# Kernel tuning notes

Hardware: AMD Instinct MI355X
Metric: run time of the kernel (lower is better)

Reference implementation:

```python
import jax, jax.numpy as jnp
import numpy as np

B, S, IN_DIM, H, NH, DH, OUT_DIM, K, N_KB, L, DFF = 32, 128, 1024, 1024, 8, 128, 256, 10, 500000, 2, 2048


def setup_inputs() -> dict:
    key = jax.random.key(0)
    ks = jax.random.split(key, 16)
    def rn(k, shape, scale=0.02):
        return jax.random.normal(k, shape, jnp.float32) * scale
    return {
        "x": jax.random.normal(ks[0], (B, S, IN_DIM), jnp.float32),
        "ctx": jax.random.normal(ks[1], (B, 1, IN_DIM), jnp.float32),
        "indices": jax.random.randint(ks[2], (B, S, K), 0, N_KB),
        "KB_embs": jax.random.normal(ks[3], (N_KB, OUT_DIM), jnp.float32),
        "W_in": rn(ks[4], (IN_DIM, H)), "b_in": jnp.zeros((H,), jnp.float32),
        "Wqkv": rn(ks[5], (L, H, 3 * H)), "bqkv": jnp.zeros((L, 3 * H), jnp.float32),
        "Wo": rn(ks[6], (L, H, H)), "bo": jnp.zeros((L, H), jnp.float32),
        "ln1_g": jnp.ones((L, H), jnp.float32), "ln1_b": jnp.zeros((L, H), jnp.float32),
        "W1": rn(ks[7], (L, H, DFF)), "b1": jnp.zeros((L, DFF), jnp.float32),
        "W2": rn(ks[8], (L, DFF, H)), "b2": jnp.zeros((L, H), jnp.float32),
        "ln2_g": jnp.ones((L, H), jnp.float32), "ln2_b": jnp.zeros((L, H), jnp.float32),
        "W_out": rn(ks[9], (H, OUT_DIM)), "b_out": jnp.zeros((OUT_DIM,), jnp.float32),
        "ds_W1": rn(ks[10], (OUT_DIM, OUT_DIM)), "ds_b1": jnp.zeros((OUT_DIM,), jnp.float32),
        "ds_W2": rn(ks[11], (OUT_DIM, 1)), "ds_b2": jnp.zeros((1,), jnp.float32),
        "cs_W1": rn(ks[12], (OUT_DIM, OUT_DIM)), "cs_b1": jnp.zeros((OUT_DIM,), jnp.float32),
        "cs_W2": rn(ks[13], (OUT_DIM, 1)), "cs_b2": jnp.zeros((1,), jnp.float32),
    }


def _ln(x, g, b, eps=1e-5):
    m = x.mean(-1, keepdims=True)
    v = ((x - m) ** 2).mean(-1, keepdims=True)
    return (x - m) * jax.lax.rsqrt(v + eps) * g + b


def _encoder_layer(h, Wqkv, bqkv, Wo, bo, g1, bn1, W1, b1, W2, b2, g2, bn2):
    # h: (Sq, Bt, H). PyTorch default batch_first=False -> axis 0 is the attended
    # sequence axis (here the data batch axis B, exactly as the original code runs).
    Sq, Bt, Hd = h.shape
    q, k, v = jnp.split(h @ Wqkv + bqkv, 3, axis=-1)
    q = q.reshape(Sq, Bt, NH, DH)
    k = k.reshape(Sq, Bt, NH, DH)
    v = v.reshape(Sq, Bt, NH, DH)
    att = jnp.einsum('sbhd,tbhd->bhst', q, k) * (1.0 / (DH ** 0.5))
    att = jax.nn.softmax(att, axis=-1)
    o = jnp.einsum('bhst,tbhd->sbhd', att, v).reshape(Sq, Bt, Hd)
    h = _ln(h + o @ Wo + bo, g1, bn1)          # post-norm, eps=1e-5
    ff = jax.nn.relu(h @ W1 + b1) @ W2 + b2    # default dim_feedforward=2048, relu
    return _ln(h + ff, g2, bn2)


def _forward(x, ctx, indices, KB_embs, W_in, b_in, Wqkv, bqkv, Wo, bo, ln1_g, ln1_b,
             W1, b1, W2, b2, ln2_g, ln2_b, W_out, b_out,
             ds_W1, ds_b1, ds_W2, ds_b2, cs_W1, cs_b1, cs_W2, cs_b2):
    h = jnp.concatenate([ctx, x], axis=1)          # (B, S+1, in_dim)
    h = jax.nn.relu(h @ W_in + b_in)               # mapper head (dropout off in eval)
    for l in range(Wqkv.shape[0]):
        h = _encoder_layer(h, Wqkv[l], bqkv[l], Wo[l], bo[l], ln1_g[l], ln1_b[l],
                           W1[l], b1[l], W2[l], b2[l], ln2_g[l], ln2_b[l])
    out = h @ W_out + b_out                        # (B, S+1, out_dim)
    ctx_e, pred = out[:, :1], out[:, 1:]
    idx = jnp.where(indices < 0, 0, indices)       # indices[indices == -1] = 0
    cand = KB_embs[idx]                            # (B, S, K, out_dim) gather
    d = cand - pred[:, :, None, :]
    c = ctx_e[:, :, None, :] * cand
    ds = jax.nn.relu(d @ ds_W1 + ds_b1) @ ds_W2 + ds_b2   # distance_score (B,S,K,1)
    cs = jax.nn.relu(c @ cs_W1 + cs_b1) @ cs_W2 + cs_b2   # context_score: computed but unused by original output
    del cs
    cand_out = jnp.concatenate([ds, cand], axis=-1)       # (B, S, K, 1+out_dim)
    return pred, cand_out


def reference(x, ctx, indices, KB_embs, W_in, b_in, Wqkv, bqkv, Wo, bo, ln1_g, ln1_b,
              W1, b1, W2, b2, ln2_g, ln2_b, W_out, b_out,
              ds_W1, ds_b1, ds_W2, ds_b2, cs_W1, cs_b1, cs_W2, cs_b2):
    return _forward(x, ctx, indices, KB_embs, W_in, b_in, Wqkv, bqkv, Wo, bo,
                    ln1_g, ln1_b, W1, b1, W2, b2, ln2_g, ln2_b, W_out, b_out,
                    ds_W1, ds_b1, ds_W2, ds_b2, cs_W1, cs_b1, cs_W2, cs_b2)
```

## Files before the change

### kernel.cpp

```cpp
#include <hip/hip_runtime.h>
#include <hip/hip_bf16.h>

typedef __attribute__((ext_vector_type(4))) float f32x4;
typedef __attribute__((ext_vector_type(8))) short s16x8;
typedef __attribute__((ext_vector_type(4))) unsigned short u16x4;

#define B_      32
#define S_      128
#define SEQ     129
#define IN_DIM  1024
#define HD      1024
#define NHEAD   8
#define DH      128
#define OUT_DIM 256
#define KC      10
#define DFF     2048
#define MROWS   (B_*SEQ)
#define MPAD    4224
#define NCAND   (B_*S_*KC)

__device__ __forceinline__ short f2bf(float f) {
  unsigned u = __builtin_bit_cast(unsigned, f);
  u += 0x7FFFu + ((u >> 16) & 1u);
  return (short)(u >> 16);
}
__device__ __forceinline__ float bf2f(short s) {
  return __builtin_bit_cast(float, ((unsigned)(unsigned short)s) << 16);
}
__device__ __forceinline__ void gload16(const short* g, short* l) {
  __builtin_amdgcn_global_load_lds(
      (const __attribute__((address_space(1))) unsigned*)g,
      (__attribute__((address_space(3))) unsigned*)l, 16, 0, 0);
}

__global__ __launch_bounds__(256) void transpose_all(
    const float* __restrict__ W_in,  const float* __restrict__ Wqkv,
    const float* __restrict__ Wo,    const float* __restrict__ W1,
    const float* __restrict__ W2,    const float* __restrict__ W_out,
    const float* __restrict__ dsW1,
    short* __restrict__ WinT,  short* __restrict__ WqkvT,
    short* __restrict__ WoT,   short* __restrict__ W1T,
    short* __restrict__ W2T,   short* __restrict__ WoutT,
    short* __restrict__ dsW1T) {
  const int b = blockIdx.x;
  const float* src; short* dst; int K, N, local;
  if (b < 1024)       { src = W_in;  dst = WinT;  K = 1024; N = 1024; local = b; }
  else if (b < 7168)  { int l = (b - 1024) / 3072; local = (b - 1024) % 3072;
                        src = Wqkv + (size_t)l * 1024 * 3072;
                        dst = WqkvT + (size_t)l * 3072 * 1024; K = 1024; N = 3072; }
  else if (b < 9216)  { int l = (b - 7168) / 1024; local = (b - 7168) % 1024;
                        src = Wo + (size_t)l * 1024 * 1024;
                        dst = WoT + (size_t)l * 1024 * 1024; K = 1024; N = 1024; }
  else if (b < 13312) { int l = (b - 9216) / 2048; local = (b - 9216) % 2048;
                        src = W1 + (size_t)l * 1024 * 2048;
                        dst = W1T + (size_t)l * 2048 * 1024; K = 1024; N = 2048; }
  else if (b < 17408) { int l = (b - 13312) / 2048; local = (b - 13312) % 2048;
                        src = W2 + (size_t)l * 2048 * 1024;
                        dst = W2T + (size_t)l * 1024 * 2048; K = 2048; N = 1024; }
  else if (b < 17664) { local = b - 17408; src = W_out; dst = WoutT; K = 1024; N = 256; }
  else                { local = b - 17664; src = dsW1;  dst = dsW1T; K = 256;  N = 256; }
  const int tilesX = N >> 5;
  const int n0 = (local % tilesX) << 5, k0 = (local / tilesX) << 5;

  __shared__ float tile[32][33];
  const int tx = threadIdx.x & 31, ty = threadIdx.x >> 5;
#pragma unroll
  for (int i = 0; i < 4; ++i)
    tile[ty + i * 8][tx] = src[(size_t)(k0 + ty + i * 8) * N + n0 + tx];
  __syncthreads();
#pragma unroll
  for (int i = 0; i < 4; ++i)
    dst[(size_t)(n0 + ty + i * 8) * K + k0 + tx] = f2bf(tile[tx][ty + i * 8]);
}

template <int EPI, bool SPLIT, typename OutT>
__global__ __launch_bounds__(256) void gemm_bt(const short* __restrict__ A,
                                               const short* __restrict__ Bt,
                                               const float* __restrict__ bias,
                                               OutT* __restrict__ C,
                                               float* __restrict__ P,
                                               int M, int N, int K,
                                               int gm, int gn, int groupM,
                                               int kper) {
  __shared__ alignas(16) short As0[4096], As1[4096];
  __shared__ alignas(16) short Bs0[4096], Bs1[4096];
  const int tid = threadIdx.x;
  const int lane = tid & 63, wave = tid >> 6;
  const int wr = wave >> 1, wc = wave & 1;

  const int nwg = gm * gn;
  int orig = blockIdx.x;
  int split = 0;
  if constexpr (SPLIT) { split = orig / nwg; orig %= nwg; }
  const int xcd = orig & 7, kk = orig >> 3;
  const int q = nwg >> 3, r = nwg & 7;
  const int wg = (xcd < r ? xcd * (q + 1) : r * (q + 1) + (xcd - r) * q) + kk;
  const int tpg = groupM * gn;
  const int grp = wg / tpg, rem = wg % tpg;
  const int g0 = grp * groupM;
  const int gsz = (groupM < gm - g0) ? groupM : (gm - g0);
  const int bm = (g0 + rem % gsz) * 128;
  const int bn = (rem / gsz) * 128;
  const int kbase = SPLIT ? split * kper : 0;

  const short* pa[2];
  const short* pb[2];
#pragma unroll
  for (int i = 0; i < 2; ++i) {
    const int idx = i * 256 + tid;
    const int rr = idx >> 2, ss = idx & 3, gg = ss ^ ((rr >> 1) & 3);
    pa[i] = A + (size_t)(bm + rr) * K + kbase + gg * 8;
    pb[i] = Bt + (size_t)(bn + rr) * K + kbase + gg * 8;
  }

  auto stage = [&](short* aBuf, short* bBuf, int t) {
    const int kofs = t << 5;
    gload16(pa[0] + kofs, aBuf + wave * 512);
    gload16(pa[1] + kofs, aBuf + 2048 + wave * 512);
    gload16(pb[0] + kofs, bBuf + wave * 512);
    gload16(pb[1] + kofs, bBuf + 2048 + wave * 512);
  };

  const int lrow = lane & 15, ks = lane >> 4;
  const int sx = (lrow >> 1) & 3;
  const int koff = ((ks ^ sx) << 3);

  f32x4 acc[4][4] = {};

  auto compute = [&](const short* as, const short* bs) {
    s16x8 af[4], bfr[4];
#pragma unroll
    for (int m = 0; m < 4; ++m)
      af[m] = *(const s16x8*)&as[(wr * 64 + m * 16 + lrow) * 32 + koff];
#pragma unroll
    for (int n = 0; n < 4; ++n)
      bfr[n] = *(const s16x8*)&bs[(wc * 64 + n * 16 + lrow) * 32 + koff];
#pragma unroll
    for (int m = 0; m < 4; ++m)
#pragma unroll
      for (int n = 0; n < 4; ++n)
        asm("v_mfma_f32_16x16x32_bf16 %0, %1, %2, %0"
            : "+v"(acc[m][n]) : "v"(af[m]), "v"(bfr[n]));
  };

  const int NT = (SPLIT ? kper : K) >> 5;
  stage(As0, Bs0, 0);
  __syncthreads();
  for (int t = 0; t < NT; t += 2) {
    stage(As1, Bs1, t + 1);
    compute(As0, Bs0);
    __syncthreads();
    if (t + 2 < NT) stage(As0, Bs0, t + 2);
    compute(As1, Bs1);
    __syncthreads();
  }

  const int lg4 = ks << 2;
#pragma unroll
  for (int n = 0; n < 4; ++n) {
    const int col = bn + wc * 64 + n * 16 + lrow;
    const float bvx = SPLIT ? 0.f : bias[col];
#pragma unroll
    for (int m = 0; m < 4; ++m) {
#pragma unroll
      for (int r2 = 0; r2 < 4; ++r2) {
        const int row = bm + wr * 64 + m * 16 + lg4 + r2;
        if constexpr (SPLIT) {
          P[((size_t)split * MPAD + row) * N + col] = acc[m][n][r2];
        } else {
          if (row < M) {
            float v = acc[m][n][r2] + bvx;
            if (EPI == 1) v = fmaxf(v, 0.f);
            if constexpr (__is_same(OutT, float)) {
              C[(size_t)row * N + col] = v;
            } else {
              C[(size_t)row * N + col] = f2bf(v);
            }
          }
        }
      }
    }
  }
}

template <int EPI, typename OutT>
__global__ __launch_bounds__(256) void reduce_cast(const float* __restrict__ P,
                                                   const float* __restrict__ bias,
                                                   OutT* __restrict__ out,
                                                   int N, int nsplit) {
  const int row = blockIdx.x;
  for (int c = threadIdx.x * 4; c < N; c += 1024) {
    f32x4 s = *(const f32x4*)(P + (size_t)row * N + c);
    for (int sp = 1; sp < nsplit; ++sp)
      s += *(const f32x4*)(P + ((size_t)sp * MPAD + row) * N + c);
    s += *(const f32x4*)(bias + c);
    if (EPI == 1) {
      s.x = fmaxf(s.x, 0.f); s.y = fmaxf(s.y, 0.f);
      s.z = fmaxf(s.z, 0.f); s.w = fmaxf(s.w, 0.f);
    }
    if constexpr (__is_same(OutT, float)) {
      *(f32x4*)(out + (size_t)row * N + c) = s;
    } else {
      u16x4 y;
      y.x = (unsigned short)f2bf(s.x); y.y = (unsigned short)f2bf(s.y);
      y.z = (unsigned short)f2bf(s.z); y.w = (unsigned short)f2bf(s.w);
      *(u16x4*)(out + (size_t)row * N + c) = y;
    }
  }
}

__global__ __launch_bounds__(256) void reduce_ln(const float* __restrict__ P,
                                                 const float* __restrict__ bias,
                                                 const float* __restrict__ g,
                                                 const float* __restrict__ bb,
                                                 short* __restrict__ h) {
  const int r = blockIdx.x, tid = threadIdx.x;
  f32x4 s = *(const f32x4*)(P + (size_t)r * 1024 + tid * 4);
  s += *(const f32x4*)(P + ((size_t)MPAD + r) * 1024 + tid * 4);
  s += *(const f32x4*)(bias + tid * 4);
  const u16x4 hv = *(const u16x4*)(h + (size_t)r * 1024 + tid * 4);
  float s0 = s.x + bf2f((short)hv.x);
  float s1 = s.y + bf2f((short)hv.y);
  float s2 = s.z + bf2f((short)hv.z);
  float s3 = s.w + bf2f((short)hv.w);
  float ls = s0 + s1 + s2 + s3;
  float l2 = s0 * s0 + s1 * s1 + s2 * s2 + s3 * s3;
#pragma unroll
  for (int off = 32; off > 0; off >>= 1) {
    ls += __shfl_down(ls, off);
    l2 += __shfl_down(l2, off);
  }
  __shared__ float red[8];
  const int wave = tid >> 6, lane = tid & 63;
  if (lane == 0) { red[wave * 2] = ls; red[wave * 2 + 1] = l2; }
  __syncthreads();
  if (tid == 0) {
    float a = 0.f, b2 = 0.f;
    for (int w = 0; w < 4; ++w) { a += red[w * 2]; b2 += red[w * 2 + 1]; }
    red[0] = a; red[1] = b2;
  }
  __syncthreads();
  const float mean = red[0] * (1.f / HD);
  const float var  = red[1] * (1.f / HD) - mean * mean;
  const float inv  = rsqrtf(var + 1e-5f);
  const f32x4 gv = *(const f32x4*)(g + tid * 4);
  const f32x4 bv = *(const f32x4*)(bb + tid * 4);
  u16x4 y;
  y.x = (unsigned short)f2bf((s0 - mean) * inv * gv.x + bv.x);
  y.y = (unsigned short)f2bf((s1 - mean) * inv * gv.y + bv.y);
  y.z = (unsigned short)f2bf((s2 - mean) * inv * gv.z + bv.z);
  y.w = (unsigned short)f2bf((s3 - mean) * inv * gv.w + bv.w);
  *(u16x4*)(h + (size_t)r * 1024 + tid * 4) = y;
}

__global__ __launch_bounds__(64) void reduce_wout(const float* __restrict__ P,
                                                  const float* __restrict__ bias,
                                                  float* __restrict__ outb,
                                                  float* __restrict__ pred) {
  const int r = blockIdx.x;
  const int c = threadIdx.x * 4;
  f32x4 s = *(const f32x4*)(P + (size_t)r * 256 + c);
  s += *(const f32x4*)(P + ((size_t)MPAD + r) * 256 + c);
  s += *(const f32x4*)(P + ((size_t)2 * MPAD + r) * 256 + c);
  s += *(const f32x4*)(P + ((size_t)3 * MPAD + r) * 256 + c);
  s += *(const f32x4*)(bias + c);
  *(f32x4*)(outb + (size_t)r * 256 + c) = s;
  const int b = r / SEQ, t = r % SEQ;
  if (t > 0) *(f32x4*)(pred + ((size_t)b * S_ + (t - 1)) * 256 + c) = s;
}

__global__ __launch_bounds__(256) void build_hin(const float* __restrict__ x,
                                                 const float* __restrict__ ctx,
                                                 short* __restrict__ hin) {
  const int r = blockIdx.x;
  const int b = r / SEQ, t = r % SEQ;
  const float* src = (t == 0) ? (ctx + (size_t)b * IN_DIM)
                              : (x + ((size_t)b * S_ + (t - 1)) * IN_DIM);
  f32x4 v = *(const f32x4*)(src + threadIdx.x * 4);
  u16x4 o;
  o.x = (unsigned short)f2bf(v.x); o.y = (unsigned short)f2bf(v.y);
  o.z = (unsigned short)f2bf(v.z); o.w = (unsigned short)f2bf(v.w);
  *(u16x4*)(hin + (size_t)r * IN_DIM + threadIdx.x * 4) = o;
}

__global__ __launch_bounds__(128) void attention_kern(const short* __restrict__ qkv,
                                                      short* __restrict__ o) {
  __shared__ alignas(16) float qs[32][132], ksm[32][132], vs[32][132];
  __shared__ float ps[32][33];
  const int t = blockIdx.x, hd = blockIdx.y, tid = threadIdx.x;
  for (int i = tid; i < 32 * 16; i += 128) {
    const int bb = i >> 4, d8 = (i & 15) << 3;
    const size_t base = (size_t)(bb * SEQ + t) * (3 * HD) + hd * DH + d8;
    s16x8 q8 = *(const s16x8*)(qkv + base);
    s16x8 k8 = *(const s16x8*)(qkv + base + HD);
    s16x8 v8 = *(const s16x8*)(qkv + base + 2 * HD);
#pragma unroll
    for (int j = 0; j < 8; ++j) {
      qs[bb][d8 + j] = bf2f(q8[j]);
      ksm[bb][d8 + j] = bf2f(k8[j]);
      vs[bb][d8 + j] = bf2f(v8[j]);
    }
  }
  __syncthreads();
  const float scale = 0.08838834764831845f;
  for (int idx = tid; idx < 1024; idx += 128) {
    const int i = idx >> 5, j = idx & 31;
    float s = 0.f;
#pragma unroll 8
    for (int d = 0; d < DH; ++d) s += qs[i][d] * ksm[j][d];
    ps[i][j] = s * scale;
  }
  __syncthreads();
  if (tid < 32) {
    float mx = -1e30f;
#pragma unroll
    for (int j = 0; j < 32; ++j) mx = fmaxf(mx, ps[tid][j]);
    float sum = 0.f;
#pragma unroll
    for (int j = 0; j < 32; ++j) { float e = __expf(ps[tid][j] - mx); ps[tid][j] = e; sum += e; }
    const float inv = 1.f / sum;
#pragma unroll
    for (int j = 0; j < 32; ++j) ps[tid][j] *= inv;
  }
  __syncthreads();
  for (int idx = tid; idx < 32 * DH; idx += 128) {
    const int i = idx >> 7, d = idx & 127;
    float s = 0.f;
#pragma unroll
    for (int j = 0; j < 32; ++j) s += ps[i][j] * vs[j][d];
    o[(size_t)(i * SEQ + t) * HD + hd * DH + d] = f2bf(s);
  }
}

__global__ __launch_bounds__(256) void cand_score(
    const float* __restrict__ outb, const int* __restrict__ indices,
    const float* __restrict__ KB, const short* __restrict__ W1T,
    const float* __restrict__ b1v, const float* __restrict__ w2v,
    const float* __restrict__ b2v, float* __restrict__ cand_out) {
  __shared__ alignas(16) short Asw[8 * 2048];
  __shared__ alignas(16) short Bs0[8192], Bs1[8192];
  __shared__ float red[64];
  const int tid = threadIdx.x;
  const int lane = tid & 63, wave = tid >> 6;
  const int lrow = lane & 15, ks = lane >> 4;
  const int sx = (lrow >> 1) & 3;
  const int koff = ((ks ^ sx) << 3);
  const int r0 = blockIdx.x << 6;

  {
    const int l4 = lane << 2;
    const int kslice = l4 >> 5, kslot = (l4 >> 3) & 3, kin = l4 & 7;
#pragma unroll
    for (int it = 0; it < 16; ++it) {
      const int rr = wave + (it << 2);
      const int R = r0 + rr;
      const int bs = R / KC, k = R - bs * KC;
      int idx = indices[(size_t)bs * KC + k];
      if (idx < 0) idx = 0;
      const int b = bs >> 7, s = bs & 127;
      f32x4 cv = *(const f32x4*)(KB + (size_t)idx * OUT_DIM + l4);
      f32x4 pv = *(const f32x4*)(outb + ((size_t)b * SEQ + s + 1) * OUT_DIM + l4);
      float* co = cand_out + (size_t)R * 257 + 1 + l4;
      co[0] = cv.x; co[1] = cv.y; co[2] = cv.z; co[3] = cv.w;
      u16x4 dv;
      dv.x = (unsigned short)f2bf(cv.x - pv.x);
      dv.y = (unsigned short)f2bf(cv.y - pv.y);
      dv.z = (unsigned short)f2bf(cv.z - pv.z);
      dv.w = (unsigned short)f2bf(cv.w - pv.w);
      const int rsw = (rr >> 1) & 3;
      *(u16x4*)&Asw[kslice * 2048 + rr * 32 + ((kslot ^ rsw) << 3) + kin] = dv;
    }
  }
  if (tid < 64) red[tid] = 0.f;

  const short* pb[4];
#pragma unroll
  for (int i = 0; i < 4; ++i) {
    const int idx2 = i * 256 + tid;
    const int rr = idx2 >> 2, ss = idx2 & 3, gg = ss ^ ((rr >> 1) & 3);
    pb[i] = W1T + (size_t)rr * 256 + gg * 8;
  }
  auto stageB = [&](short* buf, int t) {
#pragma unroll
    for (int i = 0; i < 4; ++i)
      gload16(pb[i] + (t << 5), buf + i * 2048 + wave * 512);
  };

  f32x4 acc[4][4] = {};
  auto computeDS = [&](const short* as, const short* bsrc) {
    s16x8 af[4], bfr[4];
#pragma unroll
    for (int m = 0; m < 4; ++m)
      af[m] = *(const s16x8*)&as[(m * 16 + lrow) * 32 + koff];
#pragma unroll
    for (int n = 0; n < 4; ++n)
      bfr[n] = *(const s16x8*)&bsrc[(wave * 64 + n * 16 + lrow) * 32 + koff];
#pragma unroll
    for (int m = 0; m < 4; ++m)
#pragma unroll
      for (int n = 0; n < 4; ++n)
        asm("v_mfma_f32_16x16x32_bf16 %0, %1, %2, %0"
            : "+v"(acc[m][n]) : "v"(af[m]), "v"(bfr[n]));
  };

  stageB(Bs0, 0);
  __syncthreads();
  for (int t = 0; t < 8; t += 2) {
    stageB(Bs1, t + 1);
    computeDS(Asw + t * 2048, Bs0);
    __syncthreads();
    if (t + 2 < 8) stageB(Bs0, t + 2);
    computeDS(Asw + (t + 1) * 2048, Bs1);
    __syncthreads();
  }

  float w2r[4], b1r[4];
#pragma unroll
  for (int n = 0; n < 4; ++n) {
    const int col = wave * 64 + n * 16 + lrow;
    w2r[n] = w2v[col];
    b1r[n] = b1v[col];
  }
#pragma unroll
  for (int m = 0; m < 4; ++m) {
#pragma unroll
    for (int r2 = 0; r2 < 4; ++r2) {
      float part = 0.f;
#pragma unroll
      for (int n = 0; n < 4; ++n)
        part += fmaxf(acc[m][n][r2] + b1r[n], 0.f) * w2r[n];
      part += __shfl_xor(part, 1);
      part += __shfl_xor(part, 2);
      part += __shfl_xor(part, 4);
      part += __shfl_xor(part, 8);
      if (lrow == 0) atomicAdd(&red[m * 16 + ks * 4 + r2], part);
    }
  }
  __syncthreads();
  if (tid < 64)
    cand_out[(size_t)(r0 + tid) * 257] = red[tid] + b2v[0];
}

extern "C" void kernel_launch(void* const* d_in, const int* in_sizes, int n_in,
                              void* d_out, int out_size, void* d_ws, size_t ws_size,
                              hipStream_t stream) {
  const float* x      = (const float*)d_in[0];
  const float* ctx    = (const float*)d_in[1];
  const int*   indices= (const int*)d_in[2];
  const float* KB     = (const float*)d_in[3];
  const float* W_in   = (const float*)d_in[4];
  const float* b_in   = (const float*)d_in[5];
  const float* Wqkv   = (const float*)d_in[6];
  const float* bqkv   = (const float*)d_in[7];
  const float* Wo     = (const float*)d_in[8];
  const float* bo     = (const float*)d_in[9];
  const float* ln1_g  = (const float*)d_in[10];
  const float* ln1_b  = (const float*)d_in[11];
  const float* W1     = (const float*)d_in[12];
  const float* b1     = (const float*)d_in[13];
  const float* W2     = (const float*)d_in[14];
  const float* b2     = (const float*)d_in[15];
  const float* ln2_g  = (const float*)d_in[16];
  const float* ln2_b  = (const float*)d_in[17];
  const float* W_out  = (const float*)d_in[18];
  const float* b_out  = (const float*)d_in[19];
  const float* ds_W1  = (const float*)d_in[20];
  const float* ds_b1  = (const float*)d_in[21];
  const float* ds_W2  = (const float*)d_in[22];
  const float* ds_b2  = (const float*)d_in[23];

  char* p = (char*)d_ws;
  auto alloc = [&](size_t bytes) {
    char* q = p;
    p += (bytes + 255) & ~(size_t)255;
    return q;
  };
  short* h    = (short*)alloc((size_t)MPAD * HD * 2);
  short* tmp1 = (short*)alloc((size_t)MPAD * 3 * HD * 2);
  short* tmp2 = (short*)alloc((size_t)MPAD * HD * 2);
  float* outb = (float*)alloc((size_t)MROWS * OUT_DIM * 4);
  float* part = (float*)alloc((size_t)2 * MPAD * HD * 4);
  short* WinT  = (short*)alloc((size_t)HD * IN_DIM * 2);
  short* WqkvT = (short*)alloc((size_t)2 * 3 * HD * HD * 2);
  short* WoT   = (short*)alloc((size_t)2 * HD * HD * 2);
  short* W1T   = (short*)alloc((size_t)2 * DFF * HD * 2);
  short* W2T   = (short*)alloc((size_t)2 * HD * DFF * 2);
  short* WoutT = (short*)alloc((size_t)OUT_DIM * HD * 2);
  short* dsW1T = (short*)alloc((size_t)OUT_DIM * OUT_DIM * 2);

  transpose_all<<<17728, 256, 0, stream>>>(W_in, Wqkv, Wo, W1, W2, W_out, ds_W1,
                                           WinT, WqkvT, WoT, W1T, W2T, WoutT, dsW1T);

  build_hin<<<MROWS, 256, 0, stream>>>(x, ctx, tmp2);
  gemm_bt<0, true, short><<<33 * 8 * 2, 256, 0, stream>>>(
      tmp2, WinT, nullptr, nullptr, part, MROWS, 1024, 1024, 33, 8, 8, 512);
  reduce_cast<1, short><<<MROWS, 256, 0, stream>>>(part, b_in, h, 1024, 2);

  for (int l = 0; l < 2; ++l) {
    gemm_bt<0, false, short><<<33 * 24, 256, 0, stream>>>(
        h, WqkvT + (size_t)l * 3072 * 1024, bqkv + l * 3072, tmp1, nullptr,
        MROWS, 3072, 1024, 33, 24, 8, 0);
    attention_kern<<<dim3(SEQ, NHEAD), 128, 0, stream>>>(tmp1, tmp2);
    gemm_bt<0, true, short><<<33 * 8 * 2, 256, 0, stream>>>(
        tmp2, WoT + (size_t)l * 1024 * 1024, nullptr, nullptr, part,
        MROWS, 1024, 1024, 33, 8, 8, 512);
    reduce_ln<<<MROWS, 256, 0, stream>>>(part, bo + l * 1024,
                                         ln1_g + l * 1024, ln1_b + l * 1024, h);
    gemm_bt<1, false, short><<<33 * 16, 256, 0, stream>>>(
        h, W1T + (size_t)l * 2048 * 1024, b1 + l * 2048, tmp1, nullptr,
        MROWS, 2048, 1024, 33, 16, 8, 0);
    gemm_bt<0, true, short><<<33 * 8 * 2, 256, 0, stream>>>(
        tmp1, W2T + (size_t)l * 1024 * 2048, nullptr, nullptr, part,
        MROWS, 1024, 2048, 33, 8, 4, 1024);
    reduce_ln<<<MROWS, 256, 0, stream>>>(part, b2 + l * 1024,
                                         ln2_g + l * 1024, ln2_b + l * 1024, h);
  }

  float* pred = (float*)d_out;
  float* cand_out = (float*)d_out + (size_t)B_ * S_ * OUT_DIM;

  gemm_bt<0, true, float><<<33 * 2 * 4, 256, 0, stream>>>(
      h, WoutT, nullptr, nullptr, part, MROWS, 256, 1024, 33, 2, 8, 256);
  reduce_wout<<<MROWS, 64, 0, stream>>>(part, b_out, outb, pred);

  cand_score<<<NCAND / 64, 256, 0, stream>>>(outb, indices, KB, dsW1T,
                                             ds_b1, ds_W2, ds_b2, cand_out);
}
```

Before: 511.2 us.

## Rewrite attention with bf16 MFMA, one wave per position-head pair

Replaces the scalar fp32 LDS attention kernel with one that computes QK^T and PV via 16x16x32 bf16 MFMA instructions. Each wave handles one (position, head) pair in its own LDS slice, which removes block-wide barriers and the bf16-to-fp32 conversion on load. Softmax probabilities are rounded to bf16 before the PV product, adding some precision loss.

Result: faster. 428.6 us (-16.2%).

```diff
diff --git a/kernel.cpp b/kernel.cpp
--- a/kernel.cpp
+++ b/kernel.cpp
@@ -4,6 +4,7 @@
 typedef __attribute__((ext_vector_type(4))) float f32x4;
 typedef __attribute__((ext_vector_type(8))) short s16x8;
 typedef __attribute__((ext_vector_type(4))) unsigned short u16x4;
+typedef __attribute__((ext_vector_type(8))) __bf16 bf16x8;
 
 #define B_      32
 #define S_      128
@@ -31,6 +32,10 @@
   __builtin_amdgcn_global_load_lds(
       (const __attribute__((address_space(1))) unsigned*)g,
       (__attribute__((address_space(3))) unsigned*)l, 16, 0, 0);
+}
+__device__ __forceinline__ f32x4 mfma16(s16x8 a, s16x8 b, f32x4 c) {
+  return __builtin_amdgcn_mfma_f32_16x16x32_bf16(
+      __builtin_bit_cast(bf16x8, a), __builtin_bit_cast(bf16x8, b), c, 0, 0, 0);
 }
 
 __global__ __launch_bounds__(256) void transpose_all(
@@ -283,53 +288,97 @@
   *(u16x4*)(hin + (size_t)r * IN_DIM + threadIdx.x * 4) = o;
 }
 
-__global__ __launch_bounds__(128) void attention_kern(const short* __restrict__ qkv,
+__global__ __launch_bounds__(256) void attention_mfma(const short* __restrict__ qkv,
                                                       short* __restrict__ o) {
-  __shared__ alignas(16) float qs[32][132], ksm[32][132], vs[32][132];
-  __shared__ float ps[32][33];
-  const int t = blockIdx.x, hd = blockIdx.y, tid = threadIdx.x;
-  for (int i = tid; i < 32 * 16; i += 128) {
-    const int bb = i >> 4, d8 = (i & 15) << 3;
-    const size_t base = (size_t)(bb * SEQ + t) * (3 * HD) + hd * DH + d8;
-    s16x8 q8 = *(const s16x8*)(qkv + base);
-    s16x8 k8 = *(const s16x8*)(qkv + base + HD);
-    s16x8 v8 = *(const s16x8*)(qkv + base + 2 * HD);
-#pragma unroll
-    for (int j = 0; j < 8; ++j) {
-      qs[bb][d8 + j] = bf2f(q8[j]);
-      ksm[bb][d8 + j] = bf2f(k8[j]);
-      vs[bb][d8 + j] = bf2f(v8[j]);
-    }
-  }
-  __syncthreads();
+  __shared__ alignas(16) short qs[4][32][136];
+  __shared__ alignas(16) short ksb[4][32][136];
+  __shared__ alignas(16) short vsb[4][32][136];
+  __shared__ float psb[4][32][33];
+  const int tid = threadIdx.x, lane = tid & 63, w = tid >> 6;
+  const int gw = blockIdx.x * 4 + w;
+  const int t = gw >> 3, hd = gw & 7;
+  short (*q)[136] = qs[w];
+  short (*k)[136] = ksb[w];
+  short (*v)[136] = vsb[w];
+  float (*ps)[33] = psb[w];
+
+#pragma unroll
+  for (int c = lane; c < 512; c += 64) {
+    const int bb = c >> 4, d8 = (c & 15) << 3;
+    const size_t base = ((size_t)(bb * SEQ + t)) * (3 * HD) + hd * DH + d8;
+    *(s16x8*)&q[bb][d8] = *(const s16x8*)(qkv + base);
+    *(s16x8*)&k[bb][d8] = *(const s16x8*)(qkv + base + HD);
+    *(s16x8*)&v[bb][d8] = *(const s16x8*)(qkv + base + 2 * HD);
+  }
+
+  const int lrow = lane & 15, ksl = lane >> 4;
   const float scale = 0.08838834764831845f;
-  for (int idx = tid; idx < 1024; idx += 128) {
-    const int i = idx >> 5, j = idx & 31;
-    float s = 0.f;
-#pragma unroll 8
-    for (int d = 0; d < DH; ++d) s += qs[i][d] * ksm[j][d];
-    ps[i][j] = s * scale;
-  }
-  __syncthreads();
-  if (tid < 32) {
+
+  f32x4 pacc[2][2] = {};
+#pragma unroll
+  for (int kst = 0; kst < 4; ++kst) {
+    s16x8 aq[2], bk[2];
+#pragma unroll
+    for (int m = 0; m < 2; ++m)
+      aq[m] = *(const s16x8*)&q[m * 16 + lrow][kst * 32 + ksl * 8];
+#pragma unroll
+    for (int n = 0; n < 2; ++n)
+      bk[n] = *(const s16x8*)&k[n * 16 + lrow][kst * 32 + ksl * 8];
+#pragma unroll
+    for (int m = 0; m < 2; ++m)
+#pragma unroll
+      for (int n = 0; n < 2; ++n)
+        pacc[m][n] = mfma16(aq[m], bk[n], pacc[m][n]);
+  }
+#pragma unroll
+  for (int m = 0; m < 2; ++m)
+#pragma unroll
+    for (int n = 0; n < 2; ++n)
+#pragma unroll
+      for (int r = 0; r < 4; ++r)
+        ps[m * 16 + ksl * 4 + r][n * 16 + lrow] = pacc[m][n][r] * scale;
+
+  if (lane < 32) {
     float mx = -1e30f;
 #pragma unroll
-    for (int j = 0; j < 32; ++j) mx = fmaxf(mx, ps[tid][j]);
+    for (int j = 0; j < 32; ++j) mx = fmaxf(mx, ps[lane][j]);
     float sum = 0.f;
-#pragma unroll
-    for (int j = 0; j < 32; ++j) { float e = __expf(ps[tid][j] - mx); ps[tid][j] = e; sum += e; }
+    float e[32];
+#pragma unroll
+    for (int j = 0; j < 32; ++j) { e[j] = __expf(ps[lane][j] - mx); sum += e[j]; }
     const float inv = 1.f / sum;
 #pragma unroll
-    for (int j = 0; j < 32; ++j) ps[tid][j] *= inv;
-  }
-  __syncthreads();
-  for (int idx = tid; idx < 32 * DH; idx += 128) {
-    const int i = idx >> 7, d = idx & 127;
-    float s = 0.f;
-#pragma unroll
-    for (int j = 0; j < 32; ++j) s += ps[i][j] * vs[j][d];
-    o[(size_t)(i * SEQ + t) * HD + hd * DH + d] = f2bf(s);
-  }
+    for (int j = 0; j < 32; ++j) ps[lane][j] = e[j] * inv;
+  }
+
+  s16x8 pa[2];
+#pragma unroll
+  for (int m = 0; m < 2; ++m) {
+    const float* pr = &ps[m * 16 + lrow][ksl * 8];
+#pragma unroll
+    for (int j = 0; j < 8; ++j) pa[m][j] = f2bf(pr[j]);
+  }
+  f32x4 oacc[2][8] = {};
+#pragma unroll
+  for (int n = 0; n < 8; ++n) {
+    s16x8 bv;
+#pragma unroll
+    for (int r = 0; r < 8; ++r)
+      bv[r] = v[ksl * 8 + r][n * 16 + lrow];
+#pragma unroll
+    for (int m = 0; m < 2; ++m)
+      oacc[m][n] = mfma16(pa[m], bv, oacc[m][n]);
+  }
+#pragma unroll
+  for (int m = 0; m < 2; ++m)
+#pragma unroll
+    for (int n = 0; n < 8; ++n)
+#pragma unroll
+      for (int r = 0; r < 4; ++r) {
+        const int i = m * 16 + ksl * 4 + r;
+        const int d = n * 16 + lrow;
+        o[((size_t)(i * SEQ + t)) * HD + hd * DH + d] = f2bf(oacc[m][n][r]);
+      }
 }
 
 __global__ __launch_bounds__(256) void cand_score(
@@ -500,7 +549,7 @@
     gemm_bt<0, false, short><<<33 * 24, 256, 0, stream>>>(
         h, WqkvT + (size_t)l * 3072 * 1024, bqkv + l * 3072, tmp1, nullptr,
         MROWS, 3072, 1024, 33, 24, 8, 0);
-    attention_kern<<<dim3(SEQ, NHEAD), 128, 0, stream>>>(tmp1, tmp2);
+    attention_mfma<<<258, 256, 0, stream>>>(tmp1, tmp2);
     gemm_bt<0, true, short><<<33 * 8 * 2, 256, 0, stream>>>(
         tmp2, WoT + (size_t)l * 1024 * 1024, nullptr, nullptr, part,
         MROWS, 1024, 1024, 33, 8, 8, 512);
```
